# Kernel optimization log

Hardware: AMD Instinct MI355X
Metric: run time of the kernel (lower is better)

## Reference

```python
import jax, jax.numpy as jnp
import numpy as np
import math

B, S, D, H = 2, 2048, 1024, 16
HD = D // H  # 64


def setup_inputs() -> dict:
    key = jax.random.key(0)
    ks = jax.random.split(key, 10)
    s = 1.0 / math.sqrt(D)
    return {
        "q": jax.random.normal(ks[0], (B, S, D), jnp.float32),
        "k": jax.random.normal(ks[1], (B, S, D), jnp.float32),
        "v": jax.random.normal(ks[2], (B, S, D), jnp.float32),
        "attention_mask": jnp.zeros((B, 1, 1, S), jnp.float32),
        "Wq": jax.random.normal(ks[3], (D, D), jnp.float32) * s,
        "bq": jnp.zeros((D,), jnp.float32),
        "Wk": jax.random.normal(ks[4], (D, D), jnp.float32) * s,
        "bk": jnp.zeros((D,), jnp.float32),
        "Wv": jax.random.normal(ks[5], (D, D), jnp.float32) * s,
        "bv": jnp.zeros((D,), jnp.float32),
    }


def reference(q, k, v, attention_mask, Wq, bq, Wk, bk, Wv, bv):
    # QKV projections (torch Linear: x @ W^T + b)
    def split_heads(x):  # [B,S,D] -> [B,H,S,HD]
        return x.reshape(B, S, H, HD).transpose(0, 2, 1, 3)

    ql = split_heads(q @ Wq.T + bq)
    kl = split_heads(k @ Wk.T + bk)
    vl = split_heads(v @ Wv.T + bv)

    scale = 1.0 / math.sqrt(HD)
    scores = jnp.einsum("bhqd,bhkd->bhqk", ql, kl) * scale + attention_mask
    probs = jax.nn.softmax(scores, axis=-1)  # dropout prob = 0.0 -> identity
    ctx = jnp.einsum("bhqk,bhkd->bhqd", probs, vl)
    ctx = ctx.transpose(0, 2, 1, 3).reshape(B, S, D)
    return ctx, scores
```

## Files before the change

### kernel.cpp

```cpp
#include <hip/hip_runtime.h>

typedef __bf16 bf16;
typedef __bf16 bf16x4 __attribute__((ext_vector_type(4)));
typedef __bf16 bf16x8 __attribute__((ext_vector_type(8)));
typedef float f32x4 __attribute__((ext_vector_type(4)));

#define LOG2E 1.4426950408889634f

__global__ __launch_bounds__(256, 2)
void proj_kernel(const float* __restrict__ Xq, const float* __restrict__ Xk,
                 const float* __restrict__ Xv,
                 const float* __restrict__ Wq, const float* __restrict__ Wk,
                 const float* __restrict__ Wv,
                 const float* __restrict__ Bq, const float* __restrict__ Bk,
                 const float* __restrict__ Bv,
                 bf16* __restrict__ Oq, bf16* __restrict__ Ok,
                 bf16* __restrict__ Ov)
{
    const int z = blockIdx.z;
    const float* X  = (z == 0) ? Xq : (z == 1) ? Xk : Xv;
    const float* W  = (z == 0) ? Wq : (z == 1) ? Wk : Wv;
    const float* Bi = (z == 0) ? Bq : (z == 1) ? Bk : Bv;

    const int n0 = blockIdx.x * 128;
    const int m0 = blockIdx.y * 128;

    __shared__ bf16 As[128 * 40];
    __shared__ bf16 Bs[128 * 40];

    const int t = threadIdx.x;
    const int w = t >> 6, l = t & 63, quad = l >> 4, ln = l & 15;
    const int wm = (w & 1) * 64, wn = (w >> 1) * 64;

    const f32x4 zero4 = {0.f, 0.f, 0.f, 0.f};
    f32x4 acc[4][4];
    for (int mi = 0; mi < 4; mi++)
        for (int ni = 0; ni < 4; ni++) acc[mi][ni] = zero4;

    for (int k0 = 0; k0 < 1024; k0 += 32) {
        for (int i = 0; i < 4; i++) {
            int idx = i * 256 + t;
            int row = idx >> 3, c4 = idx & 7;
            float4 a  = *(const float4*)&X[(size_t)(m0 + row) * 1024 + k0 + c4 * 4];
            float4 bb = *(const float4*)&W[(size_t)(n0 + row) * 1024 + k0 + c4 * 4];
            bf16x4 av, bv;
            av[0] = (bf16)a.x;  av[1] = (bf16)a.y;  av[2] = (bf16)a.z;  av[3] = (bf16)a.w;
            bv[0] = (bf16)bb.x; bv[1] = (bf16)bb.y; bv[2] = (bf16)bb.z; bv[3] = (bf16)bb.w;
            *(bf16x4*)&As[row * 40 + c4 * 4] = av;
            *(bf16x4*)&Bs[row * 40 + c4 * 4] = bv;
        }
        __syncthreads();

        bf16x8 af[4], bfv[4];
        for (int mi = 0; mi < 4; mi++)
            af[mi] = *(const bf16x8*)&As[(wm + mi * 16 + ln) * 40 + quad * 8];
        for (int ni = 0; ni < 4; ni++)
            bfv[ni] = *(const bf16x8*)&Bs[(wn + ni * 16 + ln) * 40 + quad * 8];
        for (int mi = 0; mi < 4; mi++)
            for (int ni = 0; ni < 4; ni++)
                acc[mi][ni] = __builtin_amdgcn_mfma_f32_16x16x32_bf16(
                    af[mi], bfv[ni], acc[mi][ni], 0, 0, 0);
        __syncthreads();
    }

    bf16* Onat = (z == 0) ? Oq : Ok;
    for (int ni = 0; ni < 4; ni++) {
        int n = n0 + wn + ni * 16 + ln;
        float bias = Bi[n];
        for (int mi = 0; mi < 4; mi++) {
            int mbase = m0 + wm + mi * 16 + quad * 4;
            if (z < 2) {
                for (int r = 0; r < 4; r++)
                    Onat[(size_t)(mbase + r) * 1024 + n] = (bf16)(acc[mi][ni][r] + bias);
            } else {
                int b = mbase >> 11, s0 = mbase & 2047;
                bf16x4 vv;
                for (int r = 0; r < 4; r++) vv[r] = (bf16)(acc[mi][ni][r] + bias);
                *(bf16x4*)&Ov[(size_t)(b * 1024 + n) * 2048 + s0] = vv;
            }
        }
    }
}

__global__ __launch_bounds__(256, 2)
void attn_kernel(const bf16* __restrict__ Qp, const bf16* __restrict__ Kp,
                 const bf16* __restrict__ Vt, const float* __restrict__ mask,
                 float* __restrict__ ctx, float* __restrict__ scores)
{
    const int qt = blockIdx.x, h = blockIdx.y, b = blockIdx.z;
    const int q0 = qt * 128;
    const int t = threadIdx.x, w = t >> 6, l = t & 63, quad = l >> 4, ln = l & 15;

    __shared__ bf16 Qs[128 * 72];
    __shared__ bf16 Ks[64 * 72];
    __shared__ bf16 VTs[64 * 72];
    __shared__ bf16 Ps[128 * 72];

    for (int i = 0; i < 4; i++) {
        int idx = i * 256 + t;
        int row = idx >> 3, d8 = idx & 7;
        *(bf16x8*)&Qs[row * 72 + d8 * 8] =
            *(const bf16x8*)&Qp[(size_t)(b * 2048 + q0 + row) * 1024 + h * 64 + d8 * 8];
    }
    __syncthreads();

    bf16x8 aq[2][2];
    for (int mi = 0; mi < 2; mi++)
        for (int ks = 0; ks < 2; ks++)
            aq[mi][ks] = *(const bf16x8*)&Qs[(w * 32 + mi * 16 + ln) * 72 + ks * 32 + quad * 8];

    const f32x4 zero4 = {0.f, 0.f, 0.f, 0.f};
    f32x4 O[2][4];
    for (int mi = 0; mi < 2; mi++)
        for (int ni = 0; ni < 4; ni++) O[mi][ni] = zero4;
    float mst[2][4], lst[2][4];
    for (int mi = 0; mi < 2; mi++)
        for (int r = 0; r < 4; r++) { mst[mi][r] = -1e30f; lst[mi][r] = 0.f; }

    const int srow_base = (b * 16 + h) * 2048 + q0 + w * 32;

    for (int kt = 0; kt < 32; kt++) {
        const int kk0 = kt * 64;
        __syncthreads();
        for (int i = 0; i < 2; i++) {
            int idx = i * 256 + t;
            int row = idx >> 3, d8 = idx & 7;
            *(bf16x8*)&Ks[row * 72 + d8 * 8] =
                *(const bf16x8*)&Kp[(size_t)(b * 2048 + kk0 + row) * 1024 + h * 64 + d8 * 8];
            *(bf16x8*)&VTs[row * 72 + d8 * 8] =
                *(const bf16x8*)&Vt[(size_t)(b * 1024 + h * 64 + row) * 2048 + kk0 + d8 * 8];
        }
        __syncthreads();

        f32x4 sa[2][4];
        for (int mi = 0; mi < 2; mi++)
            for (int ni = 0; ni < 4; ni++) sa[mi][ni] = zero4;
        for (int ks = 0; ks < 2; ks++) {
            bf16x8 kf[4];
            for (int ni = 0; ni < 4; ni++)
                kf[ni] = *(const bf16x8*)&Ks[(ni * 16 + ln) * 72 + ks * 32 + quad * 8];
            for (int mi = 0; mi < 2; mi++)
                for (int ni = 0; ni < 4; ni++)
                    sa[mi][ni] = __builtin_amdgcn_mfma_f32_16x16x32_bf16(
                        aq[mi][ks], kf[ni], sa[mi][ni], 0, 0, 0);
        }

        float maskv[4];
        for (int ni = 0; ni < 4; ni++)
            maskv[ni] = mask[b * 2048 + kk0 + ni * 16 + ln];

        float rmax[2][4];
        for (int mi = 0; mi < 2; mi++)
            for (int r = 0; r < 4; r++) rmax[mi][r] = -1e30f;
        for (int mi = 0; mi < 2; mi++) {
            for (int ni = 0; ni < 4; ni++) {
                int col = kk0 + ni * 16 + ln;
                for (int r = 0; r < 4; r++) {
                    float v = sa[mi][ni][r] * 0.125f + maskv[ni];
                    sa[mi][ni][r] = v;
                    scores[(size_t)(srow_base + mi * 16 + quad * 4 + r) * 2048 + col] = v;
                    rmax[mi][r] = fmaxf(rmax[mi][r], v);
                }
            }
        }
        for (int mi = 0; mi < 2; mi++)
            for (int r = 0; r < 4; r++) {
                float v = rmax[mi][r];
                v = fmaxf(v, __shfl_xor(v, 1));
                v = fmaxf(v, __shfl_xor(v, 2));
                v = fmaxf(v, __shfl_xor(v, 4));
                v = fmaxf(v, __shfl_xor(v, 8));
                rmax[mi][r] = v;
            }

        float alpha[2][4];
        for (int mi = 0; mi < 2; mi++)
            for (int r = 0; r < 4; r++) {
                float mnew = fmaxf(mst[mi][r], rmax[mi][r]);
                alpha[mi][r] = exp2f((mst[mi][r] - mnew) * LOG2E);
                mst[mi][r] = mnew;
            }

        float rsum[2][4];
        for (int mi = 0; mi < 2; mi++)
            for (int r = 0; r < 4; r++) rsum[mi][r] = 0.f;
        for (int mi = 0; mi < 2; mi++)
            for (int ni = 0; ni < 4; ni++)
                for (int r = 0; r < 4; r++) {
                    float p = exp2f((sa[mi][ni][r] - mst[mi][r]) * LOG2E);
                    rsum[mi][r] += p;
                    Ps[(w * 32 + mi * 16 + quad * 4 + r) * 72 + ni * 16 + ln] = (bf16)p;
                }
        for (int mi = 0; mi < 2; mi++)
            for (int r = 0; r < 4; r++) {
                float v = rsum[mi][r];
                v += __shfl_xor(v, 1);
                v += __shfl_xor(v, 2);
                v += __shfl_xor(v, 4);
                v += __shfl_xor(v, 8);
                lst[mi][r] = lst[mi][r] * alpha[mi][r] + v;
            }

        for (int mi = 0; mi < 2; mi++)
            for (int ni = 0; ni < 4; ni++)
                for (int r = 0; r < 4; r++) O[mi][ni][r] *= alpha[mi][r];

        for (int ks = 0; ks < 2; ks++) {
            bf16x8 pf[2], vf[4];
            for (int mi = 0; mi < 2; mi++)
                pf[mi] = *(const bf16x8*)&Ps[(w * 32 + mi * 16 + ln) * 72 + ks * 32 + quad * 8];
            for (int ni = 0; ni < 4; ni++)
                vf[ni] = *(const bf16x8*)&VTs[(ni * 16 + ln) * 72 + ks * 32 + quad * 8];
            for (int mi = 0; mi < 2; mi++)
                for (int ni = 0; ni < 4; ni++)
                    O[mi][ni] = __builtin_amdgcn_mfma_f32_16x16x32_bf16(
                        pf[mi], vf[ni], O[mi][ni], 0, 0, 0);
        }
    }

    for (int mi = 0; mi < 2; mi++)
        for (int ni = 0; ni < 4; ni++) {
            int n = h * 64 + ni * 16 + ln;
            for (int r = 0; r < 4; r++) {
                int row = b * 2048 + q0 + w * 32 + mi * 16 + quad * 4 + r;
                ctx[(size_t)row * 1024 + n] = O[mi][ni][r] / lst[mi][r];
            }
        }
}

extern "C" void kernel_launch(void* const* d_in, const int* in_sizes, int n_in,
                              void* d_out, int out_size, void* d_ws, size_t ws_size,
                              hipStream_t stream) {
    const float* q    = (const float*)d_in[0];
    const float* k    = (const float*)d_in[1];
    const float* v    = (const float*)d_in[2];
    const float* mask = (const float*)d_in[3];
    const float* Wq   = (const float*)d_in[4];
    const float* bq   = (const float*)d_in[5];
    const float* Wk   = (const float*)d_in[6];
    const float* bk   = (const float*)d_in[7];
    const float* Wv   = (const float*)d_in[8];
    const float* bv   = (const float*)d_in[9];

    bf16* Qp = (bf16*)d_ws;
    bf16* Kp = Qp + (size_t)4096 * 1024;
    bf16* Vt = Kp + (size_t)4096 * 1024;

    float* ctx    = (float*)d_out;
    float* scores = ctx + (size_t)2 * 2048 * 1024;

    proj_kernel<<<dim3(8, 32, 3), 256, 0, stream>>>(
        q, k, v, Wq, Wk, Wv, bq, bk, bv, Qp, Kp, Vt);
    attn_kernel<<<dim3(16, 16, 2), 256, 0, stream>>>(
        Qp, Kp, Vt, mask, ctx, scores);
}
```

Baseline: 735.1 us.

## Prefetch next tiles into registers and shrink attention query tile to 64

```diff
diff --git a/kernel.cpp b/kernel.cpp
--- a/kernel.cpp
+++ b/kernel.cpp
@@ -7,7 +7,7 @@
 
 #define LOG2E 1.4426950408889634f
 
-__global__ __launch_bounds__(256, 2)
+__global__ __launch_bounds__(256, 3)
 void proj_kernel(const float* __restrict__ Xq, const float* __restrict__ Xk,
                  const float* __restrict__ Xv,
                  const float* __restrict__ Wq, const float* __restrict__ Wk,
@@ -37,19 +37,37 @@
     for (int mi = 0; mi < 4; mi++)
         for (int ni = 0; ni < 4; ni++) acc[mi][ni] = zero4;
 
+    int srow[4], sc4[4];
+    for (int i = 0; i < 4; i++) {
+        int idx = i * 256 + t;
+        srow[i] = idx >> 3; sc4[i] = idx & 7;
+    }
+
+    float4 ra[4], rb[4];
+    for (int i = 0; i < 4; i++) {
+        ra[i] = *(const float4*)&X[(size_t)(m0 + srow[i]) * 1024 + sc4[i] * 4];
+        rb[i] = *(const float4*)&W[(size_t)(n0 + srow[i]) * 1024 + sc4[i] * 4];
+    }
+
     for (int k0 = 0; k0 < 1024; k0 += 32) {
+        if (k0) __syncthreads();
         for (int i = 0; i < 4; i++) {
-            int idx = i * 256 + t;
-            int row = idx >> 3, c4 = idx & 7;
-            float4 a  = *(const float4*)&X[(size_t)(m0 + row) * 1024 + k0 + c4 * 4];
-            float4 bb = *(const float4*)&W[(size_t)(n0 + row) * 1024 + k0 + c4 * 4];
             bf16x4 av, bv;
-            av[0] = (bf16)a.x;  av[1] = (bf16)a.y;  av[2] = (bf16)a.z;  av[3] = (bf16)a.w;
-            bv[0] = (bf16)bb.x; bv[1] = (bf16)bb.y; bv[2] = (bf16)bb.z; bv[3] = (bf16)bb.w;
-            *(bf16x4*)&As[row * 40 + c4 * 4] = av;
-            *(bf16x4*)&Bs[row * 40 + c4 * 4] = bv;
+            av[0] = (bf16)ra[i].x; av[1] = (bf16)ra[i].y;
+            av[2] = (bf16)ra[i].z; av[3] = (bf16)ra[i].w;
+            bv[0] = (bf16)rb[i].x; bv[1] = (bf16)rb[i].y;
+            bv[2] = (bf16)rb[i].z; bv[3] = (bf16)rb[i].w;
+            *(bf16x4*)&As[srow[i] * 40 + sc4[i] * 4] = av;
+            *(bf16x4*)&Bs[srow[i] * 40 + sc4[i] * 4] = bv;
         }
         __syncthreads();
+
+        if (k0 + 32 < 1024) {
+            for (int i = 0; i < 4; i++) {
+                ra[i] = *(const float4*)&X[(size_t)(m0 + srow[i]) * 1024 + k0 + 32 + sc4[i] * 4];
+                rb[i] = *(const float4*)&W[(size_t)(n0 + srow[i]) * 1024 + k0 + 32 + sc4[i] * 4];
+            }
+        }
 
         bf16x8 af[4], bfv[4];
         for (int mi = 0; mi < 4; mi++)
@@ -60,7 +78,6 @@
             for (int ni = 0; ni < 4; ni++)
                 acc[mi][ni] = __builtin_amdgcn_mfma_f32_16x16x32_bf16(
                     af[mi], bfv[ni], acc[mi][ni], 0, 0, 0);
-        __syncthreads();
     }
 
     bf16* Onat = (z == 0) ? Oq : Ok;
@@ -82,150 +99,146 @@
     }
 }
 
-__global__ __launch_bounds__(256, 2)
+__global__ __launch_bounds__(256, 4)
 void attn_kernel(const bf16* __restrict__ Qp, const bf16* __restrict__ Kp,
                  const bf16* __restrict__ Vt, const float* __restrict__ mask,
                  float* __restrict__ ctx, float* __restrict__ scores)
 {
     const int qt = blockIdx.x, h = blockIdx.y, b = blockIdx.z;
-    const int q0 = qt * 128;
+    const int q0 = qt * 64;
     const int t = threadIdx.x, w = t >> 6, l = t & 63, quad = l >> 4, ln = l & 15;
 
-    __shared__ bf16 Qs[128 * 72];
+    __shared__ bf16 Qs[64 * 72];
     __shared__ bf16 Ks[64 * 72];
     __shared__ bf16 VTs[64 * 72];
-    __shared__ bf16 Ps[128 * 72];
-
-    for (int i = 0; i < 4; i++) {
+    __shared__ bf16 Ps[64 * 72];
+
+    int srow[2], sd8[2];
+    for (int i = 0; i < 2; i++) {
         int idx = i * 256 + t;
-        int row = idx >> 3, d8 = idx & 7;
-        *(bf16x8*)&Qs[row * 72 + d8 * 8] =
-            *(const bf16x8*)&Qp[(size_t)(b * 2048 + q0 + row) * 1024 + h * 64 + d8 * 8];
+        srow[i] = idx >> 3; sd8[i] = idx & 7;
+    }
+
+    for (int i = 0; i < 2; i++)
+        *(bf16x8*)&Qs[srow[i] * 72 + sd8[i] * 8] =
+            *(const bf16x8*)&Qp[(size_t)(b * 2048 + q0 + srow[i]) * 1024 + h * 64 + sd8[i] * 8];
+
+    bf16x8 kr[2], vrr[2];
+    for (int i = 0; i < 2; i++) {
+        kr[i]  = *(const bf16x8*)&Kp[(size_t)(b * 2048 + srow[i]) * 1024 + h * 64 + sd8[i] * 8];
+        vrr[i] = *(const bf16x8*)&Vt[(size_t)(b * 1024 + h * 64 + srow[i]) * 2048 + sd8[i] * 8];
     }
     __syncthreads();
 
-    bf16x8 aq[2][2];
-    for (int mi = 0; mi < 2; mi++)
-        for (int ks = 0; ks < 2; ks++)
-            aq[mi][ks] = *(const bf16x8*)&Qs[(w * 32 + mi * 16 + ln) * 72 + ks * 32 + quad * 8];
+    bf16x8 aq[2];
+    for (int ks = 0; ks < 2; ks++)
+        aq[ks] = *(const bf16x8*)&Qs[(w * 16 + ln) * 72 + ks * 32 + quad * 8];
 
     const f32x4 zero4 = {0.f, 0.f, 0.f, 0.f};
-    f32x4 O[2][4];
-    for (int mi = 0; mi < 2; mi++)
-        for (int ni = 0; ni < 4; ni++) O[mi][ni] = zero4;
-    float mst[2][4], lst[2][4];
-    for (int mi = 0; mi < 2; mi++)
-        for (int r = 0; r < 4; r++) { mst[mi][r] = -1e30f; lst[mi][r] = 0.f; }
-
-    const int srow_base = (b * 16 + h) * 2048 + q0 + w * 32;
+    f32x4 O[4];
+    for (int ni = 0; ni < 4; ni++) O[ni] = zero4;
+    float mst[4], lst[4];
+    for (int r = 0; r < 4; r++) { mst[r] = -1e30f; lst[r] = 0.f; }
+
+    const int srow_base = (b * 16 + h) * 2048 + q0 + w * 16;
 
     for (int kt = 0; kt < 32; kt++) {
         const int kk0 = kt * 64;
+        if (kt) __syncthreads();
+        for (int i = 0; i < 2; i++) {
+            *(bf16x8*)&Ks[srow[i] * 72 + sd8[i] * 8]  = kr[i];
+            *(bf16x8*)&VTs[srow[i] * 72 + sd8[i] * 8] = vrr[i];
+        }
         __syncthreads();
-        for (int i = 0; i < 2; i++) {
-            int idx = i * 256 + t;
-            int row = idx >> 3, d8 = idx & 7;
-            *(bf16x8*)&Ks[row * 72 + d8 * 8] =
-                *(const bf16x8*)&Kp[(size_t)(b * 2048 + kk0 + row) * 1024 + h * 64 + d8 * 8];
-            *(bf16x8*)&VTs[row * 72 + d8 * 8] =
-                *(const bf16x8*)&Vt[(size_t)(b * 1024 + h * 64 + row) * 2048 + kk0 + d8 * 8];
-        }
-        __syncthreads();
-
-        f32x4 sa[2][4];
-        for (int mi = 0; mi < 2; mi++)
-            for (int ni = 0; ni < 4; ni++) sa[mi][ni] = zero4;
+
+        if (kt + 1 < 32) {
+            int kk0n = kk0 + 64;
+            for (int i = 0; i < 2; i++) {
+                kr[i]  = *(const bf16x8*)&Kp[(size_t)(b * 2048 + kk0n + srow[i]) * 1024 + h * 64 + sd8[i] * 8];
+                vrr[i] = *(const bf16x8*)&Vt[(size_t)(b * 1024 + h * 64 + srow[i]) * 2048 + kk0n + sd8[i] * 8];
+            }
+        }
+
+        f32x4 sa[4];
+        for (int ni = 0; ni < 4; ni++) sa[ni] = zero4;
         for (int ks = 0; ks < 2; ks++) {
             bf16x8 kf[4];
             for (int ni = 0; ni < 4; ni++)
                 kf[ni] = *(const bf16x8*)&Ks[(ni * 16 + ln) * 72 + ks * 32 + quad * 8];
-            for (int mi = 0; mi < 2; mi++)
-                for (int ni = 0; ni < 4; ni++)
-                    sa[mi][ni] = __builtin_amdgcn_mfma_f32_16x16x32_bf16(
-                        aq[mi][ks], kf[ni], sa[mi][ni], 0, 0, 0);
+            for (int ni = 0; ni < 4; ni++)
+                sa[ni] = __builtin_amdgcn_mfma_f32_16x16x32_bf16(
+                    aq[ks], kf[ni], sa[ni], 0, 0, 0);
         }
 
         float maskv[4];
         for (int ni = 0; ni < 4; ni++)
             maskv[ni] = mask[b * 2048 + kk0 + ni * 16 + ln];
 
-        float rmax[2][4];
-        for (int mi = 0; mi < 2; mi++)
-            for (int r = 0; r < 4; r++) rmax[mi][r] = -1e30f;
-        for (int mi = 0; mi < 2; mi++) {
-            for (int ni = 0; ni < 4; ni++) {
-                int col = kk0 + ni * 16 + ln;
-                for (int r = 0; r < 4; r++) {
-                    float v = sa[mi][ni][r] * 0.125f + maskv[ni];
-                    sa[mi][ni][r] = v;
-                    scores[(size_t)(srow_base + mi * 16 + quad * 4 + r) * 2048 + col] = v;
-                    rmax[mi][r] = fmaxf(rmax[mi][r], v);
-                }
-            }
-        }
-        for (int mi = 0; mi < 2; mi++)
+        float rmax[4];
+        for (int r = 0; r < 4; r++) rmax[r] = -1e30f;
+        for (int ni = 0; ni < 4; ni++) {
+            int col = kk0 + ni * 16 + ln;
             for (int r = 0; r < 4; r++) {
-                float v = rmax[mi][r];
-                v = fmaxf(v, __shfl_xor(v, 1));
-                v = fmaxf(v, __shfl_xor(v, 2));
-                v = fmaxf(v, __shfl_xor(v, 4));
-                v = fmaxf(v, __shfl_xor(v, 8));
-                rmax[mi][r] = v;
-            }
-
-        float alpha[2][4];
-        for (int mi = 0; mi < 2; mi++)
+                float v = sa[ni][r] * 0.125f + maskv[ni];
+                sa[ni][r] = v;
+                scores[(size_t)(srow_base + quad * 4 + r) * 2048 + col] = v;
+                rmax[r] = fmaxf(rmax[r], v);
+            }
+        }
+        for (int r = 0; r < 4; r++) {
+            float v = rmax[r];
+            v = fmaxf(v, __shfl_xor(v, 1));
+            v = fmaxf(v, __shfl_xor(v, 2));
+            v = fmaxf(v, __shfl_xor(v, 4));
+            v = fmaxf(v, __shfl_xor(v, 8));
+            rmax[r] = v;
+        }
+
+        float alpha[4];
+        for (int r = 0; r < 4; r++) {
+            float mnew = fmaxf(mst[r], rmax[r]);
+            alpha[r] = exp2f((mst[r] - mnew) * LOG2E);
+            mst[r] = mnew;
+        }
+
+        float rsum[4];
+        for (int r = 0; r < 4; r++) rsum[r] = 0.f;
+        for (int ni = 0; ni < 4; ni++)
             for (int r = 0; r < 4; r++) {
-                float mnew = fmaxf(mst[mi][r], rmax[mi][r]);
-                alpha[mi][r] = exp2f((mst[mi][r] - mnew) * LOG2E);
-                mst[mi][r] = mnew;
-            }
-
-        float rsum[2][4];
-        for (int mi = 0; mi < 2; mi++)
-            for (int r = 0; r < 4; r++) rsum[mi][r] = 0.f;
-        for (int mi = 0; mi < 2; mi++)
-            for (int ni = 0; ni < 4; ni++)
-                for (int r = 0; r < 4; r++) {
-                    float p = exp2f((sa[mi][ni][r] - mst[mi][r]) * LOG2E);
-                    rsum[mi][r] += p;
-                    Ps[(w * 32 + mi * 16 + quad * 4 + r) * 72 + ni * 16 + ln] = (bf16)p;
-                }
-        for (int mi = 0; mi < 2; mi++)
-            for (int r = 0; r < 4; r++) {
-                float v = rsum[mi][r];
-                v += __shfl_xor(v, 1);
-                v += __shfl_xor(v, 2);
-                v += __shfl_xor(v, 4);
-                v += __shfl_xor(v, 8);
-                lst[mi][r] = lst[mi][r] * alpha[mi][r] + v;
-            }
-
-        for (int mi = 0; mi < 2; mi++)
-            for (int ni = 0; ni < 4; ni++)
-                for (int r = 0; r < 4; r++) O[mi][ni][r] *= alpha[mi][r];
+                float p = exp2f((sa[ni][r] - mst[r]) * LOG2E);
+                rsum[r] += p;
+                Ps[(w * 16 + quad * 4 + r) * 72 + ni * 16 + ln] = (bf16)p;
+            }
+        for (int r = 0; r < 4; r++) {
+            float v = rsum[r];
+            v += __shfl_xor(v, 1);
+            v += __shfl_xor(v, 2);
+            v += __shfl_xor(v, 4);
+            v += __shfl_xor(v, 8);
+            lst[r] = lst[r] * alpha[r] + v;
+        }
+
+        for (int ni = 0; ni < 4; ni++)
+            for (int r = 0; r < 4; r++) O[ni][r] *= alpha[r];
 
         for (int ks = 0; ks < 2; ks++) {
-            bf16x8 pf[2], vf[4];
-            for (int mi = 0; mi < 2; mi++)
-                pf[mi] = *(const bf16x8*)&Ps[(w * 32 + mi * 16 + ln) * 72 + ks * 32 + quad * 8];
+            bf16x8 pf, vf[4];
+            pf = *(const bf16x8*)&Ps[(w * 16 + ln) * 72 + ks * 32 + quad * 8];
             for (int ni = 0; ni < 4; ni++)
                 vf[ni] = *(const bf16x8*)&VTs[(ni * 16 + ln) * 72 + ks * 32 + quad * 8];
-            for (int mi = 0; mi < 2; mi++)
-                for (int ni = 0; ni < 4; ni++)
-                    O[mi][ni] = __builtin_amdgcn_mfma_f32_16x16x32_bf16(
-                        pf[mi], vf[ni], O[mi][ni], 0, 0, 0);
-        }
-    }
-
-    for (int mi = 0; mi < 2; mi++)
-        for (int ni = 0; ni < 4; ni++) {
-            int n = h * 64 + ni * 16 + ln;
-            for (int r = 0; r < 4; r++) {
-                int row = b * 2048 + q0 + w * 32 + mi * 16 + quad * 4 + r;
-                ctx[(size_t)row * 1024 + n] = O[mi][ni][r] / lst[mi][r];
-            }
-        }
+            for (int ni = 0; ni < 4; ni++)
+                O[ni] = __builtin_amdgcn_mfma_f32_16x16x32_bf16(
+                    pf, vf[ni], O[ni], 0, 0, 0);
+        }
+    }
+
+    for (int ni = 0; ni < 4; ni++) {
+        int n = h * 64 + ni * 16 + ln;
+        for (int r = 0; r < 4; r++) {
+            int row = b * 2048 + q0 + w * 16 + quad * 4 + r;
+            ctx[(size_t)row * 1024 + n] = O[ni][r] / lst[r];
+        }
+    }
 }
 
 extern "C" void kernel_launch(void* const* d_in, const int* in_sizes, int n_in,
@@ -251,6 +264,6 @@
 
     proj_kernel<<<dim3(8, 32, 3), 256, 0, stream>>>(
         q, k, v, Wq, Wk, Wv, bq, bk, bv, Qp, Kp, Vt);
-    attn_kernel<<<dim3(16, 16, 2), 256, 0, stream>>>(
+    attn_kernel<<<dim3(32, 16, 2), 256, 0, stream>>>(
         Qp, Kp, Vt, mask, ctx, scores);
 }
```

Measured after the change: 756.9 us. +3.0%, slower.
